# Kernel optimization log

Measured on AMD Instinct MI355X. Metric: run time of the kernel, lower is better.

The kernel has to match this reference:

```python
import jax, jax.numpy as jnp
import numpy as np


def setup_inputs() -> dict:
    key = jax.random.key(0)
    ks = jax.random.split(key, 8)
    B, N, K, C_in, M, C_add, C_out = 2, 40000, 16, 64, 16, 3, 128
    in_features = (C_in + C_add) * M  # 1072
    input_features = jax.random.normal(ks[0], (B, N, C_in), dtype=jnp.float32)
    neighbor_inds = jax.random.randint(ks[1], (B, N, K), 0, N, dtype=jnp.int64)
    inverse_neighbors = jax.random.randint(ks[2], (B, N * K), 0, N * K, dtype=jnp.int64)
    inverse_k = jax.random.randint(ks[3], (B, N * K), 0, K, dtype=jnp.int64)
    inverse_idx = jax.random.randint(ks[4], (B, N * K), 0, N, dtype=jnp.int64)
    weightnet = jax.random.normal(ks[5], (B, N, K, M), dtype=jnp.float32)
    additional_features = jax.random.normal(ks[6], (B, N, K, C_add), dtype=jnp.float32)
    bound = 1.0 / np.sqrt(in_features)
    kw, kb = jax.random.split(ks[7])
    linear_weight = jax.random.uniform(kw, (C_out, in_features), dtype=jnp.float32, minval=-bound, maxval=bound)
    linear_bias = jax.random.uniform(kb, (C_out,), dtype=jnp.float32, minval=-bound, maxval=bound)
    return {
        "input_features": input_features,
        "neighbor_inds": neighbor_inds,
        "inverse_neighbors": inverse_neighbors,
        "inverse_k": inverse_k,
        "inverse_idx": inverse_idx,
        "weightnet": weightnet,
        "additional_features": additional_features,
        "linear_weight": linear_weight,
        "linear_bias": linear_bias,
    }


def reference(input_features, neighbor_inds, inverse_neighbors, inverse_k, inverse_idx,
              weightnet, additional_features, linear_weight, linear_bias):
    # inverse_* tensors are only used by the custom CUDA backward; unused here.
    B, N, K = neighbor_inds.shape
    # gather neighbor features: [B, N, K, C_in]
    gathered = jnp.take_along_axis(input_features[:, :, None, :],
                                   neighbor_inds[..., None], axis=1)
    # concat extra per-neighbor features -> [B, N, K, C]
    feats = jnp.concatenate([gathered, additional_features], axis=-1)
    # PConv: [B,N,C,K] @ [B,N,K,M] -> [B,N,C,M] -> flatten to [B,N,C*M]
    pconv = jnp.einsum('bnkc,bnkm->bncm', feats, weightnet)
    pconv = pconv.reshape(B, N, -1)
    # fused linear
    out = jnp.einsum('bnf,of->bno', pconv, linear_weight) + linear_bias
    return out
```

## Files before the change

kernel.cpp:

```cpp
#include <hip/hip_runtime.h>
#include <stdint.h>

typedef unsigned short u16;
typedef short short8 __attribute__((ext_vector_type(8)));
typedef float floatx4 __attribute__((ext_vector_type(4)));

#define NPERB   40000
#define NPTS    80000
#define KNBR    16
#define CIN     64
#define MDIM    16
#define CADD    3
#define CF      (CIN + CADD)
#define COUT    128
#define KF      1072
#define KP      1088
#define NKT     34
#define SLAB    65
#define PTSB    16

__device__ __forceinline__ u16 f2bf(float f) {
    union { float f; unsigned int u; } v; v.f = f;
    unsigned int u = v.u;
    return (u16)((u + 0x7FFFu + ((u >> 16) & 1u)) >> 16);
}
__device__ __forceinline__ short8 pack8(floatx4 x, floatx4 y) {
    union { short8 v; u16 a[8]; } u;
    u.a[0] = f2bf(x[0]); u.a[1] = f2bf(x[1]); u.a[2] = f2bf(x[2]); u.a[3] = f2bf(x[3]);
    u.a[4] = f2bf(y[0]); u.a[5] = f2bf(y[1]); u.a[6] = f2bf(y[2]); u.a[7] = f2bf(y[3]);
    return u.v;
}

__global__ void prep_lw_kernel(const float* __restrict__ lw, u16* __restrict__ lwp) {
    int i = blockIdx.x * 256 + threadIdx.x;
    if (i >= COUT * KP) return;
    int o = i / KP, f = i - o * KP;
    lwp[i] = (f < KF) ? f2bf(lw[(size_t)o * KF + f]) : (u16)0;
}

__global__ __launch_bounds__(256) void fused_kernel(
    const float* __restrict__ inp,
    const int*   __restrict__ nbr,
    const float* __restrict__ wn,
    const float* __restrict__ addl,
    const u16*   __restrict__ lwp,
    const float* __restrict__ bias,
    float* __restrict__ out)
{
    __shared__ __align__(16) u16   Apc[NKT * SLAB * 8];
    __shared__ __align__(16) float wsm[4][KNBR * MDIM];

    const int wave = threadIdx.x >> 6;
    const int lane = threadIdx.x & 63;
    const int pbase = blockIdx.x * PTSB;
    const float* inpb = inp + ((pbase >= NPERB) ? (size_t)NPERB * CIN : 0);

    for (int i = 0; i < PTSB / 4; i++) {
        const int pr = wave * 4 + i;
        const int p  = pbase + pr;

        floatx4 w4 = ((const floatx4*)(wn + (size_t)p * (KNBR * MDIM)))[lane];
        *(floatx4*)&wsm[wave][lane * 4] = w4;

        float av_hold = (lane < KNBR * CADD)
                          ? addl[(size_t)p * (KNBR * CADD) + lane] : 0.f;

        const int* nbrp = nbr + (size_t)p * KNBR;
        const floatx4* wrow = (const floatx4*)&wsm[wave][0];

        floatx4 a0 = 0, a1 = 0, a2 = 0, a3 = 0;
#pragma unroll
        for (int k = 0; k < KNBR; k++) {
            int idx = nbrp[k];
            float fv = inpb[(size_t)idx * CIN + lane];
            a0 += fv * wrow[k * 4 + 0];
            a1 += fv * wrow[k * 4 + 1];
            a2 += fv * wrow[k * 4 + 2];
            a3 += fv * wrow[k * 4 + 3];
        }
        {
            const int kt = lane >> 1, qb = (lane & 1) * 2;
            u16* ch = &Apc[(unsigned)(kt * SLAB + pr * 4 + qb) * 8];
            *(short8*)ch       = pack8(a0, a1);
            *(short8*)(ch + 8) = pack8(a2, a3);
        }

        {
            const int ec = lane >> 4, em = lane & 15;
            float ev = 0.f;
#pragma unroll
            for (int k = 0; k < KNBR; k++) {
                float av = __shfl(av_hold, k * CADD + ec);
                ev += av * wsm[wave][k * MDIM + em];
            }
            if (ec == 3) ev = 0.f;
            const int kt = 32 + (lane >> 5), quad = (lane >> 3) & 3;
            Apc[(unsigned)(kt * SLAB + pr * 4 + quad) * 8 + (lane & 7)] = f2bf(ev);
        }
    }
    __syncthreads();

    const int r16 = lane & 15, quad = lane >> 4;
    const int c0 = wave * 32;
    const u16* B0p = lwp + (size_t)(c0 + r16) * KP + quad * 8;
    const u16* B1p = B0p + (size_t)16 * KP;

    floatx4 acc0 = 0, acc1 = 0;
#pragma unroll 2
    for (int kt = 0; kt < NKT; kt++) {
        short8 A  = *(const short8*)&Apc[(unsigned)(kt * SLAB + r16 * 4 + quad) * 8];
        short8 B0 = *(const short8*)(B0p + kt * 32);
        short8 B1 = *(const short8*)(B1p + kt * 32);
        acc0 = __builtin_amdgcn_mfma_f32_16x16x32_bf16(A, B0, acc0, 0, 0, 0);
        acc1 = __builtin_amdgcn_mfma_f32_16x16x32_bf16(A, B1, acc1, 0, 0, 0);
    }

    const float bv0 = bias[c0 + r16];
    const float bv1 = bias[c0 + 16 + r16];
#pragma unroll
    for (int r = 0; r < 4; r++) {
        const size_t row = (size_t)(pbase + quad * 4 + r) * COUT;
        out[row + c0 + r16]      = acc0[r] + bv0;
        out[row + c0 + 16 + r16] = acc1[r] + bv1;
    }
}

__global__ __launch_bounds__(256) void fused_fallback_kernel(
    const float* __restrict__ inp, const int* __restrict__ nbr,
    const float* __restrict__ wn, const float* __restrict__ addl,
    const float* __restrict__ lw, const float* __restrict__ bias,
    float* __restrict__ out)
{
    const int p = blockIdx.x;
    const int b = p / NPERB;
    const int tid = threadIdx.x;
    __shared__ float sf[KNBR * CF];
    __shared__ float sw[KNBR * MDIM];
    __shared__ float sp[KF];

    sw[tid] = wn[(size_t)p * (KNBR * MDIM) + tid];
    for (int i = tid; i < KNBR * CIN; i += 256) {
        int k = i >> 6, c = i & 63;
        int idx = nbr[(size_t)p * KNBR + k];
        sf[k * CF + c] = inp[((size_t)b * NPERB + idx) * CIN + c];
    }
    if (tid < KNBR * CADD) {
        int k = tid / CADD, c = tid - k * CADD;
        sf[k * CF + CIN + c] = addl[(size_t)p * (KNBR * CADD) + tid];
    }
    __syncthreads();
    for (int f = tid; f < KF; f += 256) {
        int c = f >> 4, m = f & 15;
        float s = 0;
#pragma unroll
        for (int k = 0; k < KNBR; k++) s += sf[k * CF + c] * sw[k * MDIM + m];
        sp[f] = s;
    }
    __syncthreads();
    const int o = tid >> 1, h = tid & 1;
    float s = 0;
    for (int f = h * (KF / 2); f < (h + 1) * (KF / 2); f++)
        s += sp[f] * lw[(size_t)o * KF + f];
    s += __shfl_xor(s, 1);
    if (h == 0) out[(size_t)p * COUT + o] = s + bias[o];
}

extern "C" void kernel_launch(void* const* d_in, const int* in_sizes, int n_in,
                              void* d_out, int out_size, void* d_ws, size_t ws_size,
                              hipStream_t stream) {
    const float* inp  = (const float*)d_in[0];
    const int*   nbr  = (const int*)d_in[1];
    const float* wn   = (const float*)d_in[5];
    const float* addl = (const float*)d_in[6];
    const float* lw   = (const float*)d_in[7];
    const float* bias = (const float*)d_in[8];
    float* out = (float*)d_out;

    const size_t lw_bytes = (size_t)COUT * KP * sizeof(u16);
    if (ws_size < lw_bytes) {
        fused_fallback_kernel<<<NPTS, 256, 0, stream>>>(inp, nbr, wn, addl, lw, bias, out);
        return;
    }
    u16* lwp = (u16*)d_ws;
    prep_lw_kernel<<<(COUT * KP + 255) / 256, 256, 0, stream>>>(lw, lwp);
    fused_kernel<<<NPTS / PTSB, 256, 0, stream>>>(inp, nbr, wn, addl, lwp, bias, out);
}
```

Measured before the change: 391.3 us.

## Double points per block, drop weightnet LDS staging, and swizzle A tile

Each block now handles 32 points with 512 threads. Each wave pair splits the MFMA work by row tile and column group, so every bf16 linear-weight B tile loaded from global memory is used for two 16-row A tiles. The weightnet values are no longer staged in shared memory; each lane reads them straight from global memory, as wave-uniform vector loads and per-lane scalars. An XOR swizzle on the LDS chunk index is meant to cut bank conflicts. The risks are higher register pressure at 512 threads and redundant global weightnet reads.

After: 357.6 us. 1.09x faster.

```diff
diff --git a/kernel.cpp b/kernel.cpp
--- a/kernel.cpp
+++ b/kernel.cpp
@@ -16,8 +16,8 @@
 #define KF      1072
 #define KP      1088
 #define NKT     34
-#define SLAB    65
-#define PTSB    16
+#define PTSB    32
+#define SLAB    129
 
 __device__ __forceinline__ u16 f2bf(float f) {
     union { float f; unsigned int u; } v; v.f = f;
@@ -30,6 +30,9 @@
     u.a[4] = f2bf(y[0]); u.a[5] = f2bf(y[1]); u.a[6] = f2bf(y[2]); u.a[7] = f2bf(y[3]);
     return u.v;
 }
+__device__ __forceinline__ unsigned swz(unsigned chunk) {
+    return chunk ^ ((chunk >> 3) & 7u);
+}
 
 __global__ void prep_lw_kernel(const float* __restrict__ lw, u16* __restrict__ lwp) {
     int i = blockIdx.x * 256 + threadIdx.x;
@@ -38,7 +41,7 @@
     lwp[i] = (f < KF) ? f2bf(lw[(size_t)o * KF + f]) : (u16)0;
 }
 
-__global__ __launch_bounds__(256) void fused_kernel(
+__global__ __launch_bounds__(512) void fused_kernel(
     const float* __restrict__ inp,
     const int*   __restrict__ nbr,
     const float* __restrict__ wn,
@@ -47,68 +50,71 @@
     const float* __restrict__ bias,
     float* __restrict__ out)
 {
-    __shared__ __align__(16) u16   Apc[NKT * SLAB * 8];
-    __shared__ __align__(16) float wsm[4][KNBR * MDIM];
+    __shared__ __align__(16) u16 Apc[(NKT * SLAB + 8) * 8];
 
     const int wave = threadIdx.x >> 6;
     const int lane = threadIdx.x & 63;
     const int pbase = blockIdx.x * PTSB;
     const float* inpb = inp + ((pbase >= NPERB) ? (size_t)NPERB * CIN : 0);
 
-    for (int i = 0; i < PTSB / 4; i++) {
+    const int em = lane & 15, ec = lane >> 4;
+    for (int i = 0; i < PTSB / 8; i++) {
         const int pr = wave * 4 + i;
-        const int p  = pbase + pr;
-
-        floatx4 w4 = ((const floatx4*)(wn + (size_t)p * (KNBR * MDIM)))[lane];
-        *(floatx4*)&wsm[wave][lane * 4] = w4;
+        const int p  = __builtin_amdgcn_readfirstlane(pbase + pr);
+        const float* wp  = wn  + (size_t)p * (KNBR * MDIM);
+        const int*  nbrp = nbr + (size_t)p * KNBR;
 
         float av_hold = (lane < KNBR * CADD)
                           ? addl[(size_t)p * (KNBR * CADD) + lane] : 0.f;
 
-        const int* nbrp = nbr + (size_t)p * KNBR;
-        const floatx4* wrow = (const floatx4*)&wsm[wave][0];
+        float wv[KNBR];
+#pragma unroll
+        for (int k = 0; k < KNBR; k++) wv[k] = wp[k * MDIM + em];
 
+        {
+            float ev = 0.f;
+#pragma unroll
+            for (int k = 0; k < KNBR; k++)
+                ev += __shfl(av_hold, k * CADD + ec) * wv[k];
+            if (ec == 3) ev = 0.f;
+            unsigned kt   = 32 + (lane >> 5);
+            unsigned quad = (lane >> 3) & 3;
+            unsigned ch   = kt * SLAB + (unsigned)pr * 4 + quad;
+            Apc[swz(ch) * 8 + (lane & 7)] = f2bf(ev);
+        }
+
+        const floatx4* wp4 = (const floatx4*)wp;
         floatx4 a0 = 0, a1 = 0, a2 = 0, a3 = 0;
 #pragma unroll
         for (int k = 0; k < KNBR; k++) {
             int idx = nbrp[k];
             float fv = inpb[(size_t)idx * CIN + lane];
-            a0 += fv * wrow[k * 4 + 0];
-            a1 += fv * wrow[k * 4 + 1];
-            a2 += fv * wrow[k * 4 + 2];
-            a3 += fv * wrow[k * 4 + 3];
+            floatx4 w0 = wp4[k * 4 + 0];
+            floatx4 w1 = wp4[k * 4 + 1];
+            floatx4 w2 = wp4[k * 4 + 2];
+            floatx4 w3 = wp4[k * 4 + 3];
+            a0 += fv * w0; a1 += fv * w1; a2 += fv * w2; a3 += fv * w3;
         }
         {
-            const int kt = lane >> 1, qb = (lane & 1) * 2;
-            u16* ch = &Apc[(unsigned)(kt * SLAB + pr * 4 + qb) * 8];
-            *(short8*)ch       = pack8(a0, a1);
-            *(short8*)(ch + 8) = pack8(a2, a3);
-        }
-
-        {
-            const int ec = lane >> 4, em = lane & 15;
-            float ev = 0.f;
-#pragma unroll
-            for (int k = 0; k < KNBR; k++) {
-                float av = __shfl(av_hold, k * CADD + ec);
-                ev += av * wsm[wave][k * MDIM + em];
-            }
-            if (ec == 3) ev = 0.f;
-            const int kt = 32 + (lane >> 5), quad = (lane >> 3) & 3;
-            Apc[(unsigned)(kt * SLAB + pr * 4 + quad) * 8 + (lane & 7)] = f2bf(ev);
+            unsigned kt = lane >> 1, qb = (lane & 1) * 2;
+            unsigned ch = kt * SLAB + (unsigned)pr * 4 + qb;
+            *(short8*)&Apc[swz(ch) * 8]     = pack8(a0, a1);
+            *(short8*)&Apc[swz(ch + 1) * 8] = pack8(a2, a3);
         }
     }
     __syncthreads();
 
     const int r16 = lane & 15, quad = lane >> 4;
-    const int c0 = wave * 32;
+    const int rt = wave & 1;
+    const int c0 = (wave >> 1) * 32;
     const u16* B0p = lwp + (size_t)(c0 + r16) * KP + quad * 8;
     const u16* B1p = B0p + (size_t)16 * KP;
+    const unsigned abase = (unsigned)(rt * 16 + r16) * 4 + quad;
 
     floatx4 acc0 = 0, acc1 = 0;
 #pragma unroll 2
     for (int kt = 0; kt < NKT; kt++) {
-        short8 A  = *(const short8*)&Apc[(unsigned)(kt * SLAB + r16 * 4 + quad) * 8];
+        short8 A  = *(const short8*)&Apc[swz((unsigned)kt * SLAB + abase) * 8];
         short8 B0 = *(const short8*)(B0p + kt * 32);
         short8 B1 = *(const short8*)(B1p + kt * 32);
         acc0 = __builtin_amdgcn_mfma_f32_16x16x32_bf16(A, B0, acc0, 0, 0, 0);
@@ -119,7 +125,7 @@
     const float bv1 = bias[c0 + 16 + r16];
 #pragma unroll
     for (int r = 0; r < 4; r++) {
-        const size_t row = (size_t)(pbase + quad * 4 + r) * COUT;
+        const size_t row = (size_t)(pbase + rt * 16 + quad * 4 + r) * COUT;
         out[row + c0 + r16]      = acc0[r] + bv0;
         out[row + c0 + 16 + r16] = acc1[r] + bv1;
     }
@@ -183,5 +189,5 @@
     }
     u16* lwp = (u16*)d_ws;
     prep_lw_kernel<<<(COUT * KP + 255) / 256, 256, 0, stream>>>(lw, lwp);
-    fused_kernel<<<NPTS / PTSB, 256, 0, stream>>>(inp, nbr, wn, addl, lwp, bias, out);
+    fused_kernel<<<NPTS / PTSB, 512, 0, stream>>>(inp, nbr, wn, addl, lwp, bias, out);
 }
```
